# Performance work log

Measured on AMD Instinct MI355X. Metric: run time of the kernel, lower is better.

## Reference

```python
import jax, jax.numpy as jnp
import numpy as np

K = 20
EPS = 1e-5

def _lrelu(x):
    return jnp.where(x >= 0, x, 0.2 * x)

def _bn(x, g, b, m, v, axis=1):
    shp = [1] * x.ndim
    shp[axis] = -1
    scale = (g / jnp.sqrt(v + EPS)).reshape(shp)
    return (x - m.reshape(shp)) * scale + b.reshape(shp)

def _graph_feature(x, k):
    # x: [B, C, N] -> [B, 2C, N, k]  (kNN in feature space, concat(x_j - x_i, x_i))
    xx = jnp.sum(x * x, axis=1)                        # [B, N]
    inner = jnp.einsum('bcn,bcm->bnm', x, x)           # [B, N, N]
    neg_dist = 2.0 * inner - xx[:, :, None] - xx[:, None, :]
    _, idx = jax.lax.top_k(neg_dist, k)                # [B, N, k] nearest neighbors
    xt = jnp.transpose(x, (0, 2, 1))                   # [B, N, C]
    nb = jax.vmap(lambda f, i: f[i])(xt, idx)          # [B, N, k, C]
    center = jnp.broadcast_to(xt[:, :, None, :], nb.shape)
    feat = jnp.concatenate([nb - center, center], axis=-1)  # [B, N, k, 2C]
    return jnp.transpose(feat, (0, 3, 1, 2))

def _edge_block(x, w, g, b, m, v):
    # EdgeConv: graph feature -> 1x1 conv -> BN -> LeakyReLU -> max over k
    f = _graph_feature(x, K)                           # [B, 2C, N, k]
    y = jnp.einsum('oc,bcnk->bonk', w, f)
    y = _lrelu(_bn(y, g, b, m, v, 1))
    return jnp.max(y, axis=-1)                         # [B, O, N]


def setup_inputs() -> dict:
    key = jax.random.key(0)
    ks = iter(jax.random.split(key, 64))
    def randn(*s, scale=1.0):
        return jax.random.normal(next(ks), s, dtype=jnp.float32) * scale
    def unif(*s):
        return jax.random.uniform(next(ks), s, dtype=jnp.float32, minval=0.5, maxval=1.5)
    d = {}
    d['x'] = randn(16, 3, 1024)
    # conv / linear weights (fan-in scaled)
    for name, o, c in [('w1', 64, 6), ('w2', 64, 128), ('w3', 128, 128),
                       ('w4', 256, 256), ('w5', 1024, 512),
                       ('wl1', 512, 2048), ('wl2', 256, 512), ('wl3', 101, 256)]:
        d[name] = randn(o, c, scale=1.0 / np.sqrt(c))
    d['bl2'] = randn(256, scale=0.02)
    d['bl3'] = randn(101, scale=0.02)
    # BN params (eval-mode running stats)
    for i, c in [('1', 64), ('2', 64), ('3', 128), ('4', 256), ('5', 1024), ('6', 512), ('7', 256)]:
        d['g' + i] = 1.0 + randn(c, scale=0.1)
        d['b' + i] = randn(c, scale=0.1)
        d['m' + i] = randn(c, scale=0.1)
        d['v' + i] = unif(c)
    return d


def reference(x, w1, g1, b1, m1, v1, w2, g2, b2, m2, v2, w3, g3, b3, m3, v3,
              w4, g4, b4, m4, v4, w5, g5, b5, m5, v5,
              wl1, g6, b6, m6, v6, wl2, bl2, g7, b7, m7, v7, wl3, bl3):
    x1 = _edge_block(x,  w1, g1, b1, m1, v1)   # [B, 64, N]
    x2 = _edge_block(x1, w2, g2, b2, m2, v2)   # [B, 64, N]
    x3 = _edge_block(x2, w3, g3, b3, m3, v3)   # [B, 128, N]
    x4 = _edge_block(x3, w4, g4, b4, m4, v4)   # [B, 256, N]
    xc = jnp.concatenate([x1, x2, x3, x4], axis=1)           # [B, 512, N]
    y = _lrelu(_bn(jnp.einsum('oc,bcn->bon', w5, xc), g5, b5, m5, v5, 1))  # [B, 1024, N]
    p = jnp.concatenate([jnp.max(y, axis=-1), jnp.mean(y, axis=-1)], axis=1)  # [B, 2048]
    h = _lrelu(_bn(p @ wl1.T, g6, b6, m6, v6, 1))            # [B, 512]
    h = _lrelu(_bn(h @ wl2.T + bl2, g7, b7, m7, v7, 1))      # [B, 256]
    return h @ wl3.T + bl3                                   # [B, 101]
```

## Files before the change

kernel.cpp:

```cpp
#include <hip/hip_runtime.h>
#include <cstdint>
#include <cmath>

#define DI __device__ __forceinline__

constexpr int BB = 16;
constexpr int NN = 1024;
constexpr int KK = 20;
constexpr int NPT = BB*NN;
constexpr float EPSF = 1e-5f;
constexpr float NEGINF = -3.0e38f;

DI float lrelu(float x){ return x >= 0.f ? x : 0.2f * x; }
DI float dot4(const float4 a, const float4 b){ return a.x*b.x + a.y*b.y + a.z*b.z + a.w*b.w; }
DI unsigned short f2bf(float x){
    uint32_t u = __float_as_uint(x);
    uint32_t r = (u + 0x7fffu + ((u >> 16) & 1u)) >> 16;
    return (unsigned short)r;
}

typedef __attribute__((ext_vector_type(8))) short short8v;
typedef __attribute__((ext_vector_type(4))) float f32x4;

__global__ void k_transpose(const float* __restrict__ x, float* __restrict__ xt)
{
    int i = blockIdx.x * 256 + threadIdx.x;
    if (i >= NPT) return;
    int b = i >> 10, n = i & 1023;
    #pragma unroll
    for (int c = 0; c < 3; ++c) xt[i*3 + c] = x[(b*3 + c)*NN + n];
}

__global__ void k_sqnorm(const float* __restrict__ src, int stride, int C, float* __restrict__ xx)
{
    int i = blockIdx.x * 256 + threadIdx.x;
    if (i >= NPT) return;
    const float* r = src + (size_t)i * stride;
    float s = 0.f;
    for (int c = 0; c < C; ++c){ float v = r[c]; s += v * v; }
    xx[i] = s;
}

template<int C>
__global__ __launch_bounds__(1024, 4) void k_knn(const float* __restrict__ src, int stride,
                                                 const float* __restrict__ xx,
                                                 int* __restrict__ idxo)
{
    constexpr bool SMALL = (C == 3);
    constexpr int CG = SMALL ? 1 : (C / 4);
    constexpr int TS = SMALL ? 5 : C;
    constexpr int QS = SMALL ? 5 : C;
    __shared__ float tile[128 * TS];
    __shared__ float qbuf[64 * QS];

    const int tid  = threadIdx.x;
    const int lane = tid & 63, wave = tid >> 6;
    const int b  = blockIdx.x >> 4;
    const int q0 = (blockIdx.x & 15) << 6;
    const int qb = wave << 2;

    if constexpr (SMALL){
        for (int i = tid; i < 64*3; i += 1024){
            int row = i / 3, c = i % 3;
            qbuf[row*QS + c] = src[(size_t)(b*NN + q0 + row)*stride + c];
        }
    } else {
        for (int i = tid; i < 64*CG; i += 1024){
            int row = i / CG, cg = i % CG;
            float4 v = *(const float4*)(src + (size_t)(b*NN + q0 + row)*stride + cg*4);
            *(float4*)(qbuf + row*QS + cg*4) = v;
        }
    }

    float xxq[4];
    #pragma unroll
    for (int q = 0; q < 4; ++q) xxq[q] = xx[b*NN + q0 + qb + q];

    float val[4][16];

    #pragma unroll
    for (int t = 0; t < 8; ++t){
        __syncthreads();
        if constexpr (SMALL){
            for (int i = tid; i < 128*3; i += 1024){
                int row = i / 3, c = i % 3;
                tile[row*TS + c] = src[(size_t)(b*NN + t*128 + row)*stride + c];
            }
        } else {
            for (int i = tid; i < 128*CG; i += 1024){
                int row = i / CG, cg = i % CG;
                int p = cg ^ (row & (CG - 1));
                float4 v = *(const float4*)(src + (size_t)(b*NN + t*128 + row)*stride + cg*4);
                *(float4*)(tile + row*TS + p*4) = v;
            }
        }
        __syncthreads();

        float acc[4][2];
        #pragma unroll
        for (int q = 0; q < 4; ++q){ acc[q][0] = 0.f; acc[q][1] = 0.f; }

        if constexpr (SMALL){
            float c0a = tile[lane*TS+0], c0b = tile[lane*TS+1], c0c = tile[lane*TS+2];
            float c1a = tile[(64+lane)*TS+0], c1b = tile[(64+lane)*TS+1], c1c = tile[(64+lane)*TS+2];
            #pragma unroll
            for (int q = 0; q < 4; ++q){
                const float* qr = qbuf + (qb + q)*QS;
                float qa = qr[0], qbv = qr[1], qc = qr[2];
                acc[q][0] = qa*c0a + qbv*c0b + qc*c0c;
                acc[q][1] = qa*c1a + qbv*c1b + qc*c1c;
            }
        } else {
            const int sw = lane & (CG - 1);
            #pragma unroll 2
            for (int cg0 = 0; cg0 < CG; ++cg0){
                float4 cf0 = *(const float4*)(tile + lane*TS      + ((cg0 ^ sw) << 2));
                float4 cf1 = *(const float4*)(tile + (64+lane)*TS + ((cg0 ^ sw) << 2));
                #pragma unroll
                for (int q = 0; q < 4; ++q){
                    float4 qf = *(const float4*)(qbuf + (qb + q)*QS + (cg0 << 2));
                    acc[q][0] += dot4(qf, cf0);
                    acc[q][1] += dot4(qf, cf1);
                }
            }
        }
        float xxm0 = xx[b*NN + t*128 + lane];
        float xxm1 = xx[b*NN + t*128 + 64 + lane];
        #pragma unroll
        for (int q = 0; q < 4; ++q){
            val[q][2*t]   = 2.f*acc[q][0] - xxq[q] - xxm0;
            val[q][2*t+1] = 2.f*acc[q][1] - xxq[q] - xxm1;
        }
    }

    #pragma unroll
    for (int q = 0; q < 4; ++q){
        const int orow = (b*NN + q0 + qb + q) * KK;

        float s[16];
        #pragma unroll
        for (int j = 0; j < 16; ++j) s[j] = val[q][j];
        #pragma unroll
        for (int k = 2; k <= 16; k <<= 1){
            #pragma unroll
            for (int jj = k >> 1; jj > 0; jj >>= 1){
                #pragma unroll
                for (int i = 0; i < 16; ++i){
                    int l = i ^ jj;
                    if (l > i){
                        float a = s[i], c = s[l];
                        float mx = fmaxf(a, c), mn = fminf(a, c);
                        bool up = ((i & k) == 0);
                        s[i] = up ? mx : mn;
                        s[l] = up ? mn : mx;
                    }
                }
            }
        }

        float T = NEGINF;
        for (int it = 0; it < 21; ++it){
            float m = s[0];
            #pragma unroll
            for (int d = 1; d < 64; d <<= 1) m = fmaxf(m, __shfl_xor(m, d));
            T = m;
            unsigned long long mk = __ballot(s[0] == m);
            int wl = __ffsll(mk) - 1;
            bool adv = (lane == wl);
            #pragma unroll
            for (int j = 0; j < 15; ++j) s[j] = adv ? s[j+1] : s[j];
            s[15] = adv ? NEGINF : s[15];
        }

        int cnt = 0;
        #pragma unroll
        for (int j = 0; j < 16; ++j) cnt += (val[q][j] > T) ? 1 : 0;
        int off = cnt;
        #pragma unroll
        for (int d = 1; d < 64; d <<= 1){
            int tt = __shfl_up(off, d);
            if (lane >= d) off += tt;
        }
        int total = __shfl(off, 63);
        int pos = orow + off - cnt;
        #pragma unroll
        for (int j = 0; j < 16; ++j){
            if (val[q][j] > T){ idxo[pos] = j*64 + lane; ++pos; }
        }
        if (total < KK){
            int rem = KK - total;
            int prior = 0;
            #pragma unroll
            for (int j = 0; j < 16; ++j){
                unsigned long long mk = __ballot(val[q][j] == T);
                int below = __popcll(mk & ((1ull << lane) - 1ull));
                if ((val[q][j] == T) && (prior + below < rem))
                    idxo[orow + total + prior + below] = j*64 + lane;
                prior += __popcll(mk);
            }
        }
    }
}

__global__ void k_wprep(const float* __restrict__ w, int O, int C, float* __restrict__ wp)
{
    int i = blockIdx.x*256 + threadIdx.x;
    if (i >= O*C) return;
    int o = i / C, c = i % C;
    float a = w[o*2*C + c];
    float bq = w[o*2*C + C + c];
    wp[o*C + c]       = a;
    wp[(O + o)*C + c] = bq - a;
}

template<int K, int M2, int O>
__global__ __launch_bounds__(256) void k_uvgemm(const float* __restrict__ srcp,
    const float* __restrict__ wp,
    const float* __restrict__ g, const float* __restrict__ bp,
    const float* __restrict__ mp, const float* __restrict__ vp,
    float* __restrict__ ub, float* __restrict__ xcv)
{
    constexpr int LD = 136;
    __shared__ float wl[16*LD];
    __shared__ float xl[16*LD];
    const int tid = threadIdx.x;
    const int nt = blockIdx.x & 127;
    const int mt = blockIdx.x >> 7;
    const int to = tid >> 4, tn = tid & 15;

    float acc[8][8];
    #pragma unroll
    for (int i = 0; i < 8; ++i)
        #pragma unroll
        for (int j = 0; j < 8; ++j) acc[i][j] = 0.f;

    for (int c0 = 0; c0 < K; c0 += 16){
        __syncthreads();
        #pragma unroll
        for (int p = 0; p < 2; ++p){
            int fi = tid + (p << 8);
            int row = fi >> 2, cq = (fi & 3) << 2;
            float4 wv = *(const float4*)(wp + (size_t)(mt*128 + row)*K + c0 + cq);
            wl[(cq+0)*LD + row] = wv.x;
            wl[(cq+1)*LD + row] = wv.y;
            wl[(cq+2)*LD + row] = wv.z;
            wl[(cq+3)*LD + row] = wv.w;
            float4 xv = *(const float4*)(srcp + (size_t)(nt*128 + row)*512 + c0 + cq);
            xl[(cq+0)*LD + row] = xv.x;
            xl[(cq+1)*LD + row] = xv.y;
            xl[(cq+2)*LD + row] = xv.z;
            xl[(cq+3)*LD + row] = xv.w;
        }
        __syncthreads();
        #pragma unroll
        for (int cc = 0; cc < 16; ++cc){
            float4 a0 = *(const float4*)(wl + cc*LD + to*8);
            float4 a1 = *(const float4*)(wl + cc*LD + to*8 + 4);
            float4 b0 = *(const float4*)(xl + cc*LD + tn*8);
            float4 b1 = *(const float4*)(xl + cc*LD + tn*8 + 4);
            float av[8] = {a0.x,a0.y,a0.z,a0.w,a1.x,a1.y,a1.z,a1.w};
            float bv[8] = {b0.x,b0.y,b0.z,b0.w,b1.x,b1.y,b1.z,b1.w};
            #pragma unroll
            for (int i = 0; i < 8; ++i)
                #pragma unroll
                for (int j = 0; j < 8; ++j) acc[i][j] += av[i]*bv[j];
        }
    }

    const int mbase = mt*128 + to*8;
    const bool isu = mbase < O;
    float mult[8], add[8];
    #pragma unroll
    for (int i = 0; i < 8; ++i){
        int m = mbase + i;
        if (isu){
            float s = g[m] / sqrtf(vp[m] + EPSF);
            mult[i] = (s >= 0.f) ? 1.f : -1.f;
            add[i]  = 0.f;
        } else {
            int o = m - O;
            float s = g[o] / sqrtf(vp[o] + EPSF);
            mult[i] = s;
            add[i]  = bp[o] - mp[o]*s;
        }
    }
    #pragma unroll
    for (int j = 0; j < 8; ++j){
        int pt = nt*128 + tn*8 + j;
        float4 v0, v1;
        v0.x = fmaf(mult[0], acc[0][j], add[0]);
        v0.y = fmaf(mult[1], acc[1][j], add[1]);
        v0.z = fmaf(mult[2], acc[2][j], add[2]);
        v0.w = fmaf(mult[3], acc[3][j], add[3]);
        v1.x = fmaf(mult[4], acc[4][j], add[4]);
        v1.y = fmaf(mult[5], acc[5][j], add[5]);
        v1.z = fmaf(mult[6], acc[6][j], add[6]);
        v1.w = fmaf(mult[7], acc[7][j], add[7]);
        if (isu){
            float* d = ub + (size_t)pt*O + mbase;
            *(float4*)(d)     = v0;
            *(float4*)(d + 4) = v1;
        } else {
            float* d = xcv + (size_t)pt*512 + (mbase - O);
            *(float4*)(d)     = v0;
            *(float4*)(d + 4) = v1;
        }
    }
}

__global__ __launch_bounds__(256) void k_uv3(const float* __restrict__ xt,
    const float* __restrict__ wp,
    const float* __restrict__ g, const float* __restrict__ bp,
    const float* __restrict__ mp, const float* __restrict__ vp,
    float* __restrict__ ub, float* __restrict__ xcv)
{
    __shared__ float wpl[128*3];
    __shared__ float mult[128], add[128];
    const int tid = threadIdx.x;
    if (tid < 128){
        int m = tid;
        if (m < 64){
            float s = g[m] / sqrtf(vp[m] + EPSF);
            mult[m] = (s >= 0.f) ? 1.f : -1.f;
            add[m]  = 0.f;
        } else {
            int o = m - 64;
            float s = g[o] / sqrtf(vp[o] + EPSF);
            mult[m] = s;
            add[m]  = bp[o] - mp[o]*s;
        }
    }
    for (int i = tid; i < 128*3; i += 256) wpl[i] = wp[i];
    __syncthreads();

    const int ptl = tid >> 5, mg = tid & 31;
    const int m0 = mg * 4;
    const int pt = blockIdx.x*8 + ptl;
    float x0 = xt[pt*3+0], x1 = xt[pt*3+1], x2 = xt[pt*3+2];
    float4 v4;
    float tmp[4];
    #pragma unroll
    for (int r = 0; r < 4; ++r){
        int m = m0 + r;
        float a = wpl[m*3+0]*x0 + wpl[m*3+1]*x1 + wpl[m*3+2]*x2;
        tmp[r] = fmaf(mult[m], a, add[m]);
    }
    v4.x = tmp[0]; v4.y = tmp[1]; v4.z = tmp[2]; v4.w = tmp[3];
    if (m0 < 64) *(float4*)(ub + (size_t)pt*64 + m0) = v4;
    else         *(float4*)(xcv + (size_t)pt*512 + (m0 - 64)) = v4;
}

template<int O>
__global__ __launch_bounds__(256) void k_edgemax(const float* __restrict__ ub,
    const int* __restrict__ idxg,
    const float* __restrict__ g, const float* __restrict__ vp,
    float* __restrict__ xcv)
{
    constexpr int TPP = O / 4;
    constexpr int PPB = 256 / TPP;
    const int tid = threadIdx.x;
    const int pt  = blockIdx.x*PPB + tid / TPP;
    const int oq  = (tid % TPP) * 4;
    const int bb  = pt & ~(NN-1);

    int nb[KK];
    #pragma unroll
    for (int k = 0; k < KK; ++k) nb[k] = idxg[pt*KK + k];

    float4 mx = *(const float4*)(ub + (size_t)(bb + nb[0])*O + oq);
    #pragma unroll
    for (int k = 1; k < KK; ++k){
        float4 u = *(const float4*)(ub + (size_t)(bb + nb[k])*O + oq);
        mx.x = fmaxf(mx.x, u.x); mx.y = fmaxf(mx.y, u.y);
        mx.z = fmaxf(mx.z, u.z); mx.w = fmaxf(mx.w, u.w);
    }
    float4 gv = *(const float4*)(g + oq);
    float4 vv = *(const float4*)(vp + oq);
    float4 as;
    as.x = fabsf(gv.x / sqrtf(vv.x + EPSF));
    as.y = fabsf(gv.y / sqrtf(vv.y + EPSF));
    as.z = fabsf(gv.z / sqrtf(vv.z + EPSF));
    as.w = fabsf(gv.w / sqrtf(vv.w + EPSF));
    float* d = xcv + (size_t)pt*512 + oq;
    float4 vr = *(const float4*)(d);
    float4 y;
    y.x = lrelu(fmaf(as.x, mx.x, vr.x));
    y.y = lrelu(fmaf(as.y, mx.y, vr.y));
    y.z = lrelu(fmaf(as.z, mx.z, vr.z));
    y.w = lrelu(fmaf(as.w, mx.w, vr.w));
    *(float4*)(d) = y;
}

__global__ void k_castbf(const float* __restrict__ s, unsigned short* __restrict__ d, int n8)
{
    int i = blockIdx.x*256 + threadIdx.x;
    if (i >= n8) return;
    const float4* sp = (const float4*)s + (size_t)i*2;
    float4 a = sp[0], b = sp[1];
    union { unsigned short u[8]; uint4 v; } o;
    o.u[0] = f2bf(a.x); o.u[1] = f2bf(a.y); o.u[2] = f2bf(a.z); o.u[3] = f2bf(a.w);
    o.u[4] = f2bf(b.x); o.u[5] = f2bf(b.y); o.u[6] = f2bf(b.z); o.u[7] = f2bf(b.w);
    *((uint4*)d + i) = o.v;
}

__global__ __launch_bounds__(256) void k_conv5mfma(const unsigned short* __restrict__ xcb,
    const unsigned short* __restrict__ w5b,
    const float* __restrict__ g, const float* __restrict__ bp,
    const float* __restrict__ mp, const float* __restrict__ vp,
    float* __restrict__ pmax, float* __restrict__ psum)
{
    __shared__ __align__(16) short lA[128*32];
    __shared__ __align__(16) short lB[128*32];
    __shared__ float scl[128], adl[128];
    __shared__ float red[2][128][2];

    const int tid = threadIdx.x;
    const int lane = tid & 63, wave = tid >> 6;
    const int wm = wave >> 1, wn = wave & 1;
    const int b  = blockIdx.x >> 6;
    const int mt = (blockIdx.x >> 3) & 7;
    const int nt = blockIdx.x & 7;

    if (tid < 128){
        int o = mt*128 + tid;
        float s = g[o] / sqrtf(vp[o] + EPSF);
        scl[tid] = s;
        adl[tid] = bp[o] - mp[o]*s;
    }

    f32x4 acc[4][4];
    #pragma unroll
    for (int i = 0; i < 4; ++i)
        #pragma unroll
        for (int j = 0; j < 4; ++j) acc[i][j] = (f32x4){0.f,0.f,0.f,0.f};

    const unsigned short* gA = w5b + (size_t)(mt*128)*512;
    const unsigned short* gB = xcb + (size_t)(b*1024 + nt*128)*512;

    for (int ks = 0; ks < 16; ++ks){
        __syncthreads();
        #pragma unroll
        for (int p = 0; p < 2; ++p){
            int off = p*256 + tid;
            int row = off >> 2;
            int slot = off & 3;
            int ssl = slot ^ (row & 3);
            *(uint4*)(lA + row*32 + ssl*8) = *(const uint4*)(gA + (size_t)row*512 + ks*32 + slot*8);
            *(uint4*)(lB + row*32 + ssl*8) = *(const uint4*)(gB + (size_t)row*512 + ks*32 + slot*8);
        }
        __syncthreads();

        short8v afr[4], bfr[4];
        #pragma unroll
        for (int i = 0; i < 4; ++i){
            int row = wm*64 + i*16 + (lane & 15);
            int sl  = (lane >> 4) ^ (row & 3);
            afr[i] = *(const short8v*)(lA + row*32 + sl*8);
        }
        #pragma unroll
        for (int j = 0; j < 4; ++j){
            int row = wn*64 + j*16 + (lane & 15);
            int sl  = (lane >> 4) ^ (row & 3);
            bfr[j] = *(const short8v*)(lB + row*32 + sl*8);
        }
        #pragma unroll
        for (int i = 0; i < 4; ++i)
            #pragma unroll
            for (int j = 0; j < 4; ++j)
                acc[i][j] = __builtin_amdgcn_mfma_f32_16x16x32_bf16(afr[i], bfr[j], acc[i][j], 0, 0, 0);
    }

    float emx[4][4], esm[4][4];
    #pragma unroll
    for (int i = 0; i < 4; ++i){
        #pragma unroll
        for (int r = 0; r < 4; ++r){
            int m_loc = wm*64 + i*16 + (lane >> 4)*4 + r;
            float s = scl[m_loc], t = adl[m_loc];
            float mx = NEGINF, sm = 0.f;
            #pragma unroll
            for (int j = 0; j < 4; ++j){
                float y = lrelu(fmaf(acc[i][j][r], s, t));
                mx = fmaxf(mx, y); sm += y;
            }
            #pragma unroll
            for (int d = 1; d < 16; d <<= 1){
                mx = fmaxf(mx, __shfl_xor(mx, d));
                sm += __shfl_xor(sm, d);
            }
            emx[i][r] = mx; esm[i][r] = sm;
        }
    }
    if ((lane & 15) == 0){
        #pragma unroll
        for (int i = 0; i < 4; ++i)
            #pragma unroll
            for (int r = 0; r < 4; ++r){
                int m_loc = wm*64 + i*16 + (lane >> 4)*4 + r;
                red[wn][m_loc][0] = emx[i][r];
                red[wn][m_loc][1] = esm[i][r];
            }
    }
    __syncthreads();
    if (tid < 128){
        float mx = fmaxf(red[0][tid][0], red[1][tid][0]);
        float sm = red[0][tid][1] + red[1][tid][1];
        int o = mt*128 + tid;
        pmax[(size_t)(b*NN + o)*8 + nt] = mx;
        psum[(size_t)(b*NN + o)*8 + nt] = sm;
    }
}

__global__ void k_poolfin(const float* __restrict__ pmax, const float* __restrict__ psum,
                          float* __restrict__ p)
{
    int i = blockIdx.x*256 + threadIdx.x;
    if (i >= NPT) return;
    int b = i >> 10, o = i & 1023;
    float mx = NEGINF, sm = 0.f;
    #pragma unroll
    for (int t = 0; t < 8; ++t){ mx = fmaxf(mx, pmax[(size_t)i*8 + t]); sm += psum[(size_t)i*8 + t]; }
    p[b*2048 + o]        = mx;
    p[b*2048 + 1024 + o] = sm * (1.f/1024.f);
}

template<int IN, int O, bool HASBN, bool HASBIAS>
__global__ void k_fc(const float* __restrict__ in, const float* __restrict__ W,
                     const float* __restrict__ bias,
                     const float* __restrict__ g, const float* __restrict__ bp,
                     const float* __restrict__ mp, const float* __restrict__ vp,
                     float* __restrict__ out)
{
    int i = blockIdx.x*256 + threadIdx.x;
    if (i >= BB*O) return;
    int b = i / O, o = i % O;
    const float* wr = W  + (size_t)o*IN;
    const float* ir = in + (size_t)b*IN;
    float s = 0.f;
    #pragma unroll 4
    for (int c = 0; c < IN; c += 4){
        float4 a = *(const float4*)(wr + c);
        float4 x = *(const float4*)(ir + c);
        s += dot4(a, x);
    }
    if (HASBIAS) s += bias[o];
    if (HASBN){
        float sc = g[o] / sqrtf(vp[o] + EPSF);
        s = (s - mp[o])*sc + bp[o];
        s = lrelu(s);
    }
    out[(size_t)b*O + o] = s;
}

extern "C" void kernel_launch(void* const* d_in, const int* in_sizes, int n_in,
                              void* d_out, int out_size, void* d_ws, size_t ws_size,
                              hipStream_t stream)
{
    (void)in_sizes; (void)n_in; (void)out_size; (void)ws_size;
    const float* x   = (const float*)d_in[0];
    const float* w1  = (const float*)d_in[1];
    const float* w2  = (const float*)d_in[2];
    const float* w3  = (const float*)d_in[3];
    const float* w4  = (const float*)d_in[4];
    const float* w5  = (const float*)d_in[5];
    const float* wl1 = (const float*)d_in[6];
    const float* wl2 = (const float*)d_in[7];
    const float* wl3 = (const float*)d_in[8];
    const float* bl2 = (const float*)d_in[9];
    const float* bl3 = (const float*)d_in[10];
    const float* g1 = (const float*)d_in[11]; const float* b1 = (const float*)d_in[12];
    const float* m1 = (const float*)d_in[13]; const float* v1 = (const float*)d_in[14];
    const float* g2 = (const float*)d_in[15]; const float* b2 = (const float*)d_in[16];
    const float* m2 = (const float*)d_in[17]; const float* v2 = (const float*)d_in[18];
    const float* g3 = (const float*)d_in[19]; const float* b3 = (const float*)d_in[20];
    const float* m3 = (const float*)d_in[21]; const float* v3 = (const float*)d_in[22];
    const float* g4 = (const float*)d_in[23]; const float* b4 = (const float*)d_in[24];
    const float* m4 = (const float*)d_in[25]; const float* v4 = (const float*)d_in[26];
    const float* g5 = (const float*)d_in[27]; const float* b5 = (const float*)d_in[28];
    const float* m5 = (const float*)d_in[29]; const float* v5 = (const float*)d_in[30];
    const float* g6 = (const float*)d_in[31]; const float* b6 = (const float*)d_in[32];
    const float* m6 = (const float*)d_in[33]; const float* v6 = (const float*)d_in[34];
    const float* g7 = (const float*)d_in[35]; const float* b7 = (const float*)d_in[36];
    const float* m7 = (const float*)d_in[37]; const float* v7 = (const float*)d_in[38];

    float* wsf  = (float*)d_ws;
    float* xt0  = wsf;
    float* xc   = xt0 + 49152;
    float* xx   = xc + 8388608;
    int*   idx  = (int*)(xx + 16384);
    float* pmax = (float*)(idx + 327680);
    float* psum = pmax + 131072;
    float* p    = psum + 131072;
    float* h1   = p + 32768;
    float* h2   = h1 + 8192;
    float* ub   = h2 + 4096;
    float* wp   = ub + 4194304;
    unsigned short* xcb = (unsigned short*)ub;
    unsigned short* w5b = (unsigned short*)idx;

    k_transpose<<<64, 256, 0, stream>>>(x, xt0);

    k_sqnorm<<<64, 256, 0, stream>>>(xt0, 3, 3, xx);
    k_knn<3><<<256, 1024, 0, stream>>>(xt0, 3, xx, idx);
    k_wprep<<<1, 256, 0, stream>>>(w1, 64, 3, wp);
    k_uv3<<<2048, 256, 0, stream>>>(xt0, wp, g1, b1, m1, v1, ub, xc);
    k_edgemax<64><<<1024, 256, 0, stream>>>(ub, idx, g1, v1, xc);

    k_sqnorm<<<64, 256, 0, stream>>>(xc, 512, 64, xx);
    k_knn<64><<<256, 1024, 0, stream>>>(xc, 512, xx, idx);
    k_wprep<<<16, 256, 0, stream>>>(w2, 64, 64, wp);
    k_uvgemm<64, 128, 64><<<128, 256, 0, stream>>>(xc, wp, g2, b2, m2, v2, ub, xc + 64);
    k_edgemax<64><<<1024, 256, 0, stream>>>(ub, idx, g2, v2, xc + 64);

    k_sqnorm<<<64, 256, 0, stream>>>(xc + 64, 512, 64, xx);
    k_knn<64><<<256, 1024, 0, stream>>>(xc + 64, 512, xx, idx);
    k_wprep<<<32, 256, 0, stream>>>(w3, 128, 64, wp);
    k_uvgemm<64, 256, 128><<<256, 256, 0, stream>>>(xc + 64, wp, g3, b3, m3, v3, ub, xc + 128);
    k_edgemax<128><<<2048, 256, 0, stream>>>(ub, idx, g3, v3, xc + 128);

    k_sqnorm<<<64, 256, 0, stream>>>(xc + 128, 512, 128, xx);
    k_knn<128><<<256, 1024, 0, stream>>>(xc + 128, 512, xx, idx);
    k_wprep<<<128, 256, 0, stream>>>(w4, 256, 128, wp);
    k_uvgemm<128, 512, 256><<<512, 256, 0, stream>>>(xc + 128, wp, g4, b4, m4, v4, ub, xc + 256);
    k_edgemax<256><<<4096, 256, 0, stream>>>(ub, idx, g4, v4, xc + 256);

    k_castbf<<<4096, 256, 0, stream>>>(xc, xcb, 1048576);
    k_castbf<<<256, 256, 0, stream>>>(w5, w5b, 65536);
    k_conv5mfma<<<1024, 256, 0, stream>>>(xcb, w5b, g5, b5, m5, v5, pmax, psum);
    k_poolfin<<<64, 256, 0, stream>>>(pmax, psum, p);

    k_fc<2048, 512, true,  false><<<32, 256, 0, stream>>>(p,  wl1, nullptr, g6, b6, m6, v6, h1);
    k_fc<512,  256, true,  true ><<<16, 256, 0, stream>>>(h1, wl2, bl2,     g7, b7, m7, v7, h2);
    k_fc<256,  101, false, true ><<<7,  256, 0, stream>>>(h2, wl3, bl3, nullptr, nullptr, nullptr, nullptr, (float*)d_out);
}
```

Measured before the change: 650.4 us.

## Restructure kNN distance kernel to chunk channels and stage all candidates in LDS

The kNN kernel now loads all 1024 candidate points into shared memory, 8 channels at a time, and accumulates partial dot products across channel chunks. Query features stay in registers instead of a shared buffer. Blocks shrink to 512 threads handling 32 queries, and the grid doubles to 512. The aim is fewer barriers per candidate and better occupancy and LDS use. The cost is that query rows are reloaded from global memory for every chunk, and the padded 12-float row stride may cause LDS bank conflicts.

```diff
diff --git a/kernel.cpp b/kernel.cpp
--- a/kernel.cpp
+++ b/kernel.cpp
@@ -42,100 +42,97 @@
 }
 
 template<int C>
-__global__ __launch_bounds__(1024, 4) void k_knn(const float* __restrict__ src, int stride,
-                                                 const float* __restrict__ xx,
-                                                 int* __restrict__ idxo)
+__global__ __launch_bounds__(512, 4) void k_knn(const float* __restrict__ src, int stride,
+                                                const float* __restrict__ xx,
+                                                int* __restrict__ idxo)
 {
     constexpr bool SMALL = (C == 3);
-    constexpr int CG = SMALL ? 1 : (C / 4);
-    constexpr int TS = SMALL ? 5 : C;
-    constexpr int QS = SMALL ? 5 : C;
-    __shared__ float tile[128 * TS];
-    __shared__ float qbuf[64 * QS];
+    constexpr int NCH = SMALL ? 1 : (C / 8);
+    constexpr int RS  = SMALL ? 4 : 12;
+    __shared__ float tile[1024 * RS];
 
     const int tid  = threadIdx.x;
-    const int lane = tid & 63, wave = tid >> 6;
-    const int b  = blockIdx.x >> 4;
-    const int q0 = (blockIdx.x & 15) << 6;
-    const int qb = wave << 2;
-
-    if constexpr (SMALL){
-        for (int i = tid; i < 64*3; i += 1024){
-            int row = i / 3, c = i % 3;
-            qbuf[row*QS + c] = src[(size_t)(b*NN + q0 + row)*stride + c];
-        }
-    } else {
-        for (int i = tid; i < 64*CG; i += 1024){
-            int row = i / CG, cg = i % CG;
-            float4 v = *(const float4*)(src + (size_t)(b*NN + q0 + row)*stride + cg*4);
-            *(float4*)(qbuf + row*QS + cg*4) = v;
-        }
-    }
-
-    float xxq[4];
-    #pragma unroll
-    for (int q = 0; q < 4; ++q) xxq[q] = xx[b*NN + q0 + qb + q];
+    const int lane = tid & 63;
+    const int wv   = __builtin_amdgcn_readfirstlane(tid >> 6);
+    const int b    = blockIdx.x >> 5;
+    const int q0   = (blockIdx.x & 31) << 5;
+    const int qbase = b*NN + q0 + (wv << 2);
 
     float val[4][16];
-
-    #pragma unroll
-    for (int t = 0; t < 8; ++t){
+    #pragma unroll
+    for (int q = 0; q < 4; ++q)
+        #pragma unroll
+        for (int j = 0; j < 16; ++j) val[q][j] = 0.f;
+
+    for (int ch = 0; ch < NCH; ++ch){
+        const int c0 = ch << 3;
         __syncthreads();
         if constexpr (SMALL){
-            for (int i = tid; i < 128*3; i += 1024){
-                int row = i / 3, c = i % 3;
-                tile[row*TS + c] = src[(size_t)(b*NN + t*128 + row)*stride + c];
+            #pragma unroll
+            for (int r = 0; r < 2; ++r){
+                int c = tid*2 + r;
+                const float* sp = src + (size_t)(b*NN + c)*3;
+                float4 v; v.x = sp[0]; v.y = sp[1]; v.z = sp[2]; v.w = 0.f;
+                *(float4*)(tile + c*4) = v;
             }
         } else {
-            for (int i = tid; i < 128*CG; i += 1024){
-                int row = i / CG, cg = i % CG;
-                int p = cg ^ (row & (CG - 1));
-                float4 v = *(const float4*)(src + (size_t)(b*NN + t*128 + row)*stride + cg*4);
-                *(float4*)(tile + row*TS + p*4) = v;
+            #pragma unroll
+            for (int k = 0; k < 4; ++k){
+                int id = tid + k*512;
+                int c = id >> 1, part = id & 1;
+                float4 v = *(const float4*)(src + (size_t)(b*NN + c)*stride + c0 + part*4);
+                *(float4*)(tile + c*12 + part*4) = v;
+            }
+        }
+        float4 qa[4], qb4[4];
+        if constexpr (SMALL){
+            #pragma unroll
+            for (int q = 0; q < 4; ++q){
+                const float* qp = src + (size_t)(qbase + q)*3;
+                qa[q].x = qp[0]; qa[q].y = qp[1]; qa[q].z = qp[2]; qa[q].w = 0.f;
+            }
+        } else {
+            #pragma unroll
+            for (int q = 0; q < 4; ++q){
+                const float* qp = src + (size_t)(qbase + q)*stride + c0;
+                qa[q]  = *(const float4*)(qp);
+                qb4[q] = *(const float4*)(qp + 4);
             }
         }
         __syncthreads();
 
-        float acc[4][2];
-        #pragma unroll
-        for (int q = 0; q < 4; ++q){ acc[q][0] = 0.f; acc[q][1] = 0.f; }
-
-        if constexpr (SMALL){
-            float c0a = tile[lane*TS+0], c0b = tile[lane*TS+1], c0c = tile[lane*TS+2];
-            float c1a = tile[(64+lane)*TS+0], c1b = tile[(64+lane)*TS+1], c1c = tile[(64+lane)*TS+2];
-            #pragma unroll
-            for (int q = 0; q < 4; ++q){
-                const float* qr = qbuf + (qb + q)*QS;
-                float qa = qr[0], qbv = qr[1], qc = qr[2];
-                acc[q][0] = qa*c0a + qbv*c0b + qc*c0c;
-                acc[q][1] = qa*c1a + qbv*c1b + qc*c1c;
-            }
-        } else {
-            const int sw = lane & (CG - 1);
-            #pragma unroll 2
-            for (int cg0 = 0; cg0 < CG; ++cg0){
-                float4 cf0 = *(const float4*)(tile + lane*TS      + ((cg0 ^ sw) << 2));
-                float4 cf1 = *(const float4*)(tile + (64+lane)*TS + ((cg0 ^ sw) << 2));
+        #pragma unroll
+        for (int j = 0; j < 16; ++j){
+            if constexpr (SMALL){
+                float4 cf = *(const float4*)(tile + (size_t)(j*64 + lane)*4);
                 #pragma unroll
-                for (int q = 0; q < 4; ++q){
-                    float4 qf = *(const float4*)(qbuf + (qb + q)*QS + (cg0 << 2));
-                    acc[q][0] += dot4(qf, cf0);
-                    acc[q][1] += dot4(qf, cf1);
-                }
-            }
-        }
-        float xxm0 = xx[b*NN + t*128 + lane];
-        float xxm1 = xx[b*NN + t*128 + 64 + lane];
-        #pragma unroll
-        for (int q = 0; q < 4; ++q){
-            val[q][2*t]   = 2.f*acc[q][0] - xxq[q] - xxm0;
-            val[q][2*t+1] = 2.f*acc[q][1] - xxq[q] - xxm1;
-        }
+                for (int q = 0; q < 4; ++q)
+                    val[q][j] += qa[q].x*cf.x + qa[q].y*cf.y + qa[q].z*cf.z;
+            } else {
+                const float* cp = tile + (size_t)(j*64 + lane)*12;
+                float4 cf0 = *(const float4*)(cp);
+                float4 cf1 = *(const float4*)(cp + 4);
+                #pragma unroll
+                for (int q = 0; q < 4; ++q)
+                    val[q][j] += dot4(qa[q], cf0) + dot4(qb4[q], cf1);
+            }
+        }
+    }
+
+    float xxq[4];
+    #pragma unroll
+    for (int q = 0; q < 4; ++q) xxq[q] = xx[qbase + q];
+    #pragma unroll
+    for (int j = 0; j < 16; ++j){
+        float xm = xx[b*NN + j*64 + lane];
+        #pragma unroll
+        for (int q = 0; q < 4; ++q)
+            val[q][j] = 2.f*val[q][j] - xxq[q] - xm;
     }
 
     #pragma unroll
     for (int q = 0; q < 4; ++q){
-        const int orow = (b*NN + q0 + qb + q) * KK;
+        const int orow = (qbase + q) * KK;
 
         float s[16];
         #pragma unroll
@@ -601,25 +598,25 @@
     k_transpose<<<64, 256, 0, stream>>>(x, xt0);
 
     k_sqnorm<<<64, 256, 0, stream>>>(xt0, 3, 3, xx);
-    k_knn<3><<<256, 1024, 0, stream>>>(xt0, 3, xx, idx);
+    k_knn<3><<<512, 512, 0, stream>>>(xt0, 3, xx, idx);
     k_wprep<<<1, 256, 0, stream>>>(w1, 64, 3, wp);
     k_uv3<<<2048, 256, 0, stream>>>(xt0, wp, g1, b1, m1, v1, ub, xc);
     k_edgemax<64><<<1024, 256, 0, stream>>>(ub, idx, g1, v1, xc);
 
     k_sqnorm<<<64, 256, 0, stream>>>(xc, 512, 64, xx);
-    k_knn<64><<<256, 1024, 0, stream>>>(xc, 512, xx, idx);
+    k_knn<64><<<512, 512, 0, stream>>>(xc, 512, xx, idx);
     k_wprep<<<16, 256, 0, stream>>>(w2, 64, 64, wp);
     k_uvgemm<64, 128, 64><<<128, 256, 0, stream>>>(xc, wp, g2, b2, m2, v2, ub, xc + 64);
     k_edgemax<64><<<1024, 256, 0, stream>>>(ub, idx, g2, v2, xc + 64);
 
     k_sqnorm<<<64, 256, 0, stream>>>(xc + 64, 512, 64, xx);
-    k_knn<64><<<256, 1024, 0, stream>>>(xc + 64, 512, xx, idx);
+    k_knn<64><<<512, 512, 0, stream>>>(xc + 64, 512, xx, idx);
     k_wprep<<<32, 256, 0, stream>>>(w3, 128, 64, wp);
     k_uvgemm<64, 256, 128><<<256, 256, 0, stream>>>(xc + 64, wp, g3, b3, m3, v3, ub, xc + 128);
     k_edgemax<128><<<2048, 256, 0, stream>>>(ub, idx, g3, v3, xc + 128);
 
     k_sqnorm<<<64, 256, 0, stream>>>(xc + 128, 512, 128, xx);
-    k_knn<128><<<256, 1024, 0, stream>>>(xc + 128, 512, xx, idx);
+    k_knn<128><<<512, 512, 0, stream>>>(xc + 128, 512, xx, idx);
     k_wprep<<<128, 256, 0, stream>>>(w4, 256, 128, wp);
     k_uvgemm<128, 512, 256><<<512, 256, 0, stream>>>(xc + 128, wp, g4, b4, m4, v4, ub, xc + 256);
     k_edgemax<256><<<4096, 256, 0, stream>>>(ub, idx, g4, v4, xc + 256);
```

Result: slower. 1.522 ms (+134.0%).

## Rework kNN kernel: 8 queries per wave, wave-uniform query loads, paired top-k selection

Applied to the files above, without the earlier changes.

The kNN kernel now uses 512-thread blocks with 8 waves, and each wave handles 8 query rows instead of 4. Query rows are read straight from global memory through wave-uniform pointers (readfirstlane), which should become scalar loads, and the shared query buffer is removed. Each candidate tile is reused across twice as many queries. The bitonic sort and 21-step wave-max selection now process two queries together to interleave shuffle latency. The cost is more registers per thread (val is now 8x16) and fewer waves per block, which may reduce occupancy.

```diff
diff --git a/kernel.cpp b/kernel.cpp
--- a/kernel.cpp
+++ b/kernel.cpp
@@ -42,52 +42,42 @@
 }
 
 template<int C>
-__global__ __launch_bounds__(1024, 4) void k_knn(const float* __restrict__ src, int stride,
-                                                 const float* __restrict__ xx,
-                                                 int* __restrict__ idxo)
+__global__ __launch_bounds__(512, 2) void k_knn(const float* __restrict__ src, int stride,
+                                                const float* __restrict__ xx,
+                                                int* __restrict__ idxo)
 {
     constexpr bool SMALL = (C == 3);
     constexpr int CG = SMALL ? 1 : (C / 4);
     constexpr int TS = SMALL ? 5 : C;
-    constexpr int QS = SMALL ? 5 : C;
     __shared__ float tile[128 * TS];
-    __shared__ float qbuf[64 * QS];
 
     const int tid  = threadIdx.x;
-    const int lane = tid & 63, wave = tid >> 6;
+    const int lane = tid & 63;
+    const int wv   = __builtin_amdgcn_readfirstlane(tid >> 6);
     const int b  = blockIdx.x >> 4;
     const int q0 = (blockIdx.x & 15) << 6;
-    const int qb = wave << 2;
-
-    if constexpr (SMALL){
-        for (int i = tid; i < 64*3; i += 1024){
-            int row = i / 3, c = i % 3;
-            qbuf[row*QS + c] = src[(size_t)(b*NN + q0 + row)*stride + c];
-        }
-    } else {
-        for (int i = tid; i < 64*CG; i += 1024){
-            int row = i / CG, cg = i % CG;
-            float4 v = *(const float4*)(src + (size_t)(b*NN + q0 + row)*stride + cg*4);
-            *(float4*)(qbuf + row*QS + cg*4) = v;
-        }
-    }
-
-    float xxq[4];
-    #pragma unroll
-    for (int q = 0; q < 4; ++q) xxq[q] = xx[b*NN + q0 + qb + q];
-
-    float val[4][16];
+    const int qbase = b*NN + q0 + (wv << 3);
+
+    const float* qp[8];
+    #pragma unroll
+    for (int q = 0; q < 8; ++q) qp[q] = src + (size_t)(qbase + q)*stride;
+
+    float xxq[8];
+    #pragma unroll
+    for (int q = 0; q < 8; ++q) xxq[q] = xx[qbase + q];
+
+    float val[8][16];
 
     #pragma unroll
     for (int t = 0; t < 8; ++t){
         __syncthreads();
         if constexpr (SMALL){
-            for (int i = tid; i < 128*3; i += 1024){
+            for (int i = tid; i < 128*3; i += 512){
                 int row = i / 3, c = i % 3;
                 tile[row*TS + c] = src[(size_t)(b*NN + t*128 + row)*stride + c];
             }
         } else {
-            for (int i = tid; i < 128*CG; i += 1024){
+            for (int i = tid; i < 128*CG; i += 512){
                 int row = i / CG, cg = i % CG;
                 int p = cg ^ (row & (CG - 1));
                 float4 v = *(const float4*)(src + (size_t)(b*NN + t*128 + row)*stride + cg*4);
@@ -96,50 +86,47 @@
         }
         __syncthreads();
 
-        float acc[4][2];
-        #pragma unroll
-        for (int q = 0; q < 4; ++q){ acc[q][0] = 0.f; acc[q][1] = 0.f; }
+        float acc0[8], acc1[8];
+        #pragma unroll
+        for (int q = 0; q < 8; ++q){ acc0[q] = 0.f; acc1[q] = 0.f; }
 
         if constexpr (SMALL){
             float c0a = tile[lane*TS+0], c0b = tile[lane*TS+1], c0c = tile[lane*TS+2];
             float c1a = tile[(64+lane)*TS+0], c1b = tile[(64+lane)*TS+1], c1c = tile[(64+lane)*TS+2];
             #pragma unroll
-            for (int q = 0; q < 4; ++q){
-                const float* qr = qbuf + (qb + q)*QS;
-                float qa = qr[0], qbv = qr[1], qc = qr[2];
-                acc[q][0] = qa*c0a + qbv*c0b + qc*c0c;
-                acc[q][1] = qa*c1a + qbv*c1b + qc*c1c;
+            for (int q = 0; q < 8; ++q){
+                float qa = qp[q][0], qb = qp[q][1], qc = qp[q][2];
+                acc0[q] = qa*c0a + qb*c0b + qc*c0c;
+                acc1[q] = qa*c1a + qb*c1b + qc*c1c;
             }
         } else {
             const int sw = lane & (CG - 1);
-            #pragma unroll 2
             for (int cg0 = 0; cg0 < CG; ++cg0){
                 float4 cf0 = *(const float4*)(tile + lane*TS      + ((cg0 ^ sw) << 2));
                 float4 cf1 = *(const float4*)(tile + (64+lane)*TS + ((cg0 ^ sw) << 2));
                 #pragma unroll
-                for (int q = 0; q < 4; ++q){
-                    float4 qf = *(const float4*)(qbuf + (qb + q)*QS + (cg0 << 2));
-                    acc[q][0] += dot4(qf, cf0);
-                    acc[q][1] += dot4(qf, cf1);
+                for (int q = 0; q < 8; ++q){
+                    float4 qf = *(const float4*)(qp[q] + (cg0 << 2));
+                    acc0[q] += dot4(qf, cf0);
+                    acc1[q] += dot4(qf, cf1);
                 }
             }
         }
         float xxm0 = xx[b*NN + t*128 + lane];
         float xxm1 = xx[b*NN + t*128 + 64 + lane];
         #pragma unroll
-        for (int q = 0; q < 4; ++q){
-            val[q][2*t]   = 2.f*acc[q][0] - xxq[q] - xxm0;
-            val[q][2*t+1] = 2.f*acc[q][1] - xxq[q] - xxm1;
-        }
-    }
-
-    #pragma unroll
-    for (int q = 0; q < 4; ++q){
-        const int orow = (b*NN + q0 + qb + q) * KK;
-
-        float s[16];
-        #pragma unroll
-        for (int j = 0; j < 16; ++j) s[j] = val[q][j];
+        for (int q = 0; q < 8; ++q){
+            val[q][2*t]   = 2.f*acc0[q] - xxq[q] - xxm0;
+            val[q][2*t+1] = 2.f*acc1[q] - xxq[q] - xxm1;
+        }
+    }
+
+    #pragma unroll
+    for (int qq = 0; qq < 8; qq += 2){
+        float s0[16], s1[16];
+        #pragma unroll
+        for (int j = 0; j < 16; ++j){ s0[j] = val[qq][j]; s1[j] = val[qq+1][j]; }
+
         #pragma unroll
         for (int k = 2; k <= 16; k <<= 1){
             #pragma unroll
@@ -148,55 +135,73 @@
                 for (int i = 0; i < 16; ++i){
                     int l = i ^ jj;
                     if (l > i){
-                        float a = s[i], c = s[l];
-                        float mx = fmaxf(a, c), mn = fminf(a, c);
                         bool up = ((i & k) == 0);
-                        s[i] = up ? mx : mn;
-                        s[l] = up ? mn : mx;
+                        float a0 = s0[i], c0 = s0[l];
+                        float mx0 = fmaxf(a0, c0), mn0 = fminf(a0, c0);
+                        s0[i] = up ? mx0 : mn0;  s0[l] = up ? mn0 : mx0;
+                        float a1 = s1[i], c1 = s1[l];
+                        float mx1 = fmaxf(a1, c1), mn1 = fminf(a1, c1);
+                        s1[i] = up ? mx1 : mn1;  s1[l] = up ? mn1 : mx1;
                     }
                 }
             }
         }
 
-        float T = NEGINF;
+        float T0 = NEGINF, T1 = NEGINF;
         for (int it = 0; it < 21; ++it){
-            float m = s[0];
-            #pragma unroll
-            for (int d = 1; d < 64; d <<= 1) m = fmaxf(m, __shfl_xor(m, d));
-            T = m;
-            unsigned long long mk = __ballot(s[0] == m);
-            int wl = __ffsll(mk) - 1;
-            bool adv = (lane == wl);
-            #pragma unroll
-            for (int j = 0; j < 15; ++j) s[j] = adv ? s[j+1] : s[j];
-            s[15] = adv ? NEGINF : s[15];
-        }
-
-        int cnt = 0;
-        #pragma unroll
-        for (int j = 0; j < 16; ++j) cnt += (val[q][j] > T) ? 1 : 0;
-        int off = cnt;
-        #pragma unroll
-        for (int d = 1; d < 64; d <<= 1){
-            int tt = __shfl_up(off, d);
-            if (lane >= d) off += tt;
-        }
-        int total = __shfl(off, 63);
-        int pos = orow + off - cnt;
-        #pragma unroll
-        for (int j = 0; j < 16; ++j){
-            if (val[q][j] > T){ idxo[pos] = j*64 + lane; ++pos; }
-        }
-        if (total < KK){
-            int rem = KK - total;
-            int prior = 0;
+            float m0 = s0[0], m1 = s1[0];
+            #pragma unroll
+            for (int d = 1; d < 64; d <<= 1){
+                float p0 = __shfl_xor(m0, d);
+                float p1 = __shfl_xor(m1, d);
+                m0 = fmaxf(m0, p0);
+                m1 = fmaxf(m1, p1);
+            }
+            T0 = m0; T1 = m1;
+            unsigned long long mk0 = __ballot(s0[0] == m0);
+            unsigned long long mk1 = __ballot(s1[0] == m1);
+            bool a0 = (lane == __ffsll(mk0) - 1);
+            bool a1 = (lane == __ffsll(mk1) - 1);
+            #pragma unroll
+            for (int j = 0; j < 15; ++j){
+                s0[j] = a0 ? s0[j+1] : s0[j];
+                s1[j] = a1 ? s1[j+1] : s1[j];
+            }
+            s0[15] = a0 ? NEGINF : s0[15];
+            s1[15] = a1 ? NEGINF : s1[15];
+        }
+
+        #pragma unroll
+        for (int h = 0; h < 2; ++h){
+            const int q = qq + h;
+            const float T = h ? T1 : T0;
+            const int orow = (qbase + q) * KK;
+            int cnt = 0;
+            #pragma unroll
+            for (int j = 0; j < 16; ++j) cnt += (val[q][j] > T) ? 1 : 0;
+            int off = cnt;
+            #pragma unroll
+            for (int d = 1; d < 64; d <<= 1){
+                int tt = __shfl_up(off, d);
+                if (lane >= d) off += tt;
+            }
+            int total = __shfl(off, 63);
+            int pos = orow + off - cnt;
             #pragma unroll
             for (int j = 0; j < 16; ++j){
-                unsigned long long mk = __ballot(val[q][j] == T);
-                int below = __popcll(mk & ((1ull << lane) - 1ull));
-                if ((val[q][j] == T) && (prior + below < rem))
-                    idxo[orow + total + prior + below] = j*64 + lane;
-                prior += __popcll(mk);
+                if (val[q][j] > T){ idxo[pos] = j*64 + lane; ++pos; }
+            }
+            if (total < KK){
+                int rem = KK - total;
+                int prior = 0;
+                #pragma unroll
+                for (int j = 0; j < 16; ++j){
+                    unsigned long long mk = __ballot(val[q][j] == T);
+                    int below = __popcll(mk & ((1ull << lane) - 1ull));
+                    if ((val[q][j] == T) && (prior + below < rem))
+                        idxo[orow + total + prior + below] = j*64 + lane;
+                    prior += __popcll(mk);
+                }
             }
         }
     }
@@ -601,25 +606,25 @@
     k_transpose<<<64, 256, 0, stream>>>(x, xt0);
 
     k_sqnorm<<<64, 256, 0, stream>>>(xt0, 3, 3, xx);
-    k_knn<3><<<256, 1024, 0, stream>>>(xt0, 3, xx, idx);
+    k_knn<3><<<256, 512, 0, stream>>>(xt0, 3, xx, idx);
     k_wprep<<<1, 256, 0, stream>>>(w1, 64, 3, wp);
     k_uv3<<<2048, 256, 0, stream>>>(xt0, wp, g1, b1, m1, v1, ub, xc);
     k_edgemax<64><<<1024, 256, 0, stream>>>(ub, idx, g1, v1, xc);
 
     k_sqnorm<<<64, 256, 0, stream>>>(xc, 512, 64, xx);
-    k_knn<64><<<256, 1024, 0, stream>>>(xc, 512, xx, idx);
+    k_knn<64><<<256, 512, 0, stream>>>(xc, 512, xx, idx);
     k_wprep<<<16, 256, 0, stream>>>(w2, 64, 64, wp);
     k_uvgemm<64, 128, 64><<<128, 256, 0, stream>>>(xc, wp, g2, b2, m2, v2, ub, xc + 64);
     k_edgemax<64><<<1024, 256, 0, stream>>>(ub, idx, g2, v2, xc + 64);
 
     k_sqnorm<<<64, 256, 0, stream>>>(xc + 64, 512, 64, xx);
-    k_knn<64><<<256, 1024, 0, stream>>>(xc + 64, 512, xx, idx);
+    k_knn<64><<<256, 512, 0, stream>>>(xc + 64, 512, xx, idx);
     k_wprep<<<32, 256, 0, stream>>>(w3, 128, 64, wp);
     k_uvgemm<64, 256, 128><<<256, 256, 0, stream>>>(xc + 64, wp, g3, b3, m3, v3, ub, xc + 128);
     k_edgemax<128><<<2048, 256, 0, stream>>>(ub, idx, g3, v3, xc + 128);
 
     k_sqnorm<<<64, 256, 0, stream>>>(xc + 128, 512, 128, xx);
-    k_knn<128><<<256, 1024, 0, stream>>>(xc + 128, 512, xx, idx);
+    k_knn<128><<<256, 512, 0, stream>>>(xc + 128, 512, xx, idx);
     k_wprep<<<128, 256, 0, stream>>>(w4, 256, 128, wp);
     k_uvgemm<128, 512, 256><<<512, 256, 0, stream>>>(xc + 128, wp, g4, b4, m4, v4, ub, xc + 256);
     k_edgemax<256><<<4096, 256, 0, stream>>>(ub, idx, g4, v4, xc + 256);
```

Measured after the change: 740.4 us. 13.9% more time.
